# Kernel optimization log

Hardware: AMD Instinct MI355X
Metric: run time of the kernel (lower is better)

The kernel has to match this reference:

```python
import jax, jax.numpy as jnp
import numpy as np

# --- vocab metadata (replaces string itos_vocab lookups with precomputed tables) ---
# ids [0,128)   : pitch    'p0'..'p127'  (type 0)
# ids [128,289) : duration 'd0'..'d160'  (type 1)
# ids [289,390) : time     't0'..'t100'  (type 2)
# ids [390,518) : velocity 'v0'..'v127'  (type 3)
_tt = np.concatenate([np.full(128, 0), np.full(161, 1), np.full(101, 2), np.full(128, 3)]).astype(np.int32)
_tv = np.concatenate([np.arange(128), np.arange(161), np.arange(101), np.arange(128)]).astype(np.float32)
TOKEN_TYPE = jnp.asarray(_tt)   # [V]
TOKEN_VALUE = jnp.asarray(_tv)  # [V]
COEF = (1.0, 0.5, 0.5, 0.5, 0.5)  # matches init coeff_
# per-type numeric-distance normalizers (pitch unused: its branch is constant)
DENOM = jnp.array([1.0, 160.0, 100.0, 128.0], dtype=jnp.float32)
CW = jnp.array([COEF[1], COEF[2], COEF[3], COEF[4]], dtype=jnp.float32)

B, V, S = 32, 518, 2048


def setup_inputs() -> dict:
    key = jax.random.key(0)
    k1, k2 = jax.random.split(key)
    output = jax.random.normal(k1, (B, V, S), dtype=jnp.float32)  # logits [B, vocab, S]
    target = jax.random.randint(k2, (B, S), 0, V, dtype=jnp.int64)
    return {"output": output, "target": target}


def reference(output, target):
    target = target.astype(jnp.int32)
    # CrossEntropyLoss over class dim 1, mean over B*S
    lsm = jax.nn.log_softmax(output, axis=1)                       # [B,V,S]
    nll = -jnp.take_along_axis(lsm, target[:, None, :], axis=1)    # [B,1,S]
    loss = nll.mean()
    # faithful to source: softmax over last (sequence) dim, then argmax over vocab dim
    pred = jnp.argmax(jax.nn.softmax(output, axis=-1), axis=1)     # [B,S]
    pt, tt = TOKEN_TYPE[pred], TOKEN_TYPE[target]
    pv, tv = TOKEN_VALUE[pred], TOKEN_VALUE[target]
    diff = jnp.abs(pv - tv)
    # pitch branch: source compares 'pXX' != 'XX' which is always True -> constant coef[1]
    same_type = jnp.where(pt == 0, COEF[1], CW[pt] * diff / DENOM[pt])
    mask = jnp.where(pt != tt, COEF[0], same_type)                 # [B,S]
    high_cost = (loss * mask).mean()
    return loss + high_cost
```

## Files before the change

kernel.cpp:

```cpp
#include <hip/hip_runtime.h>

#define BV 518
#define SS 2048
#define NB 32
#define NCOL (NB * SS)

__device__ inline void tok_meta(int id, int& ty, float& val) {
    int base;
    if (id < 128)      { ty = 0; base = 0; }
    else if (id < 289) { ty = 1; base = 128; }
    else if (id < 390) { ty = 2; base = 289; }
    else               { ty = 3; base = 390; }
    val = (float)(id - base);
}

__global__ __launch_bounds__(256) void row_lse_kernel(const float* __restrict__ logits,
                                                      float* __restrict__ lse_row) {
    const int row = blockIdx.x;
    const float4* base4 = (const float4*)(logits + (size_t)row * SS);
    const int t = threadIdx.x;
    float4 x0 = base4[t];
    float4 x1 = base4[t + 256];
    float s = __expf(x0.x) + __expf(x0.y) + __expf(x0.z) + __expf(x0.w)
            + __expf(x1.x) + __expf(x1.y) + __expf(x1.z) + __expf(x1.w);
    #pragma unroll
    for (int off = 32; off; off >>= 1) s += __shfl_down(s, off);
    __shared__ float ws[4];
    if ((t & 63) == 0) ws[t >> 6] = s;
    __syncthreads();
    if (t == 0) lse_row[row] = __logf(ws[0] + ws[1] + ws[2] + ws[3]);
}

__global__ __launch_bounds__(256) void col_partial_kernel(const float* __restrict__ logits,
                                                          const float* __restrict__ lse_row,
                                                          float* __restrict__ pse,
                                                          float* __restrict__ pbs,
                                                          int*   __restrict__ pbi) {
    const int bid   = blockIdx.x;
    const int vh    = bid >> 8;
    const int b     = (bid >> 3) & 31;
    const int stile = bid & 7;
    const int t     = threadIdx.x;
    const int lane  = t & 63;
    const int part  = t >> 6;

    __shared__ float slse[BV];
    for (int i = t; i < BV; i += 256) slse[i] = lse_row[b * BV + i];
    __syncthreads();

    const int fidx = stile * 64 + lane;
    const float4* rowbase = (const float4*)(logits + (size_t)b * BV * SS);

    const int vbase = vh ? 259 : 0;
    const int vend  = vh ? BV  : 259;

    float4 se = make_float4(0.f, 0.f, 0.f, 0.f);
    float4 bs = make_float4(-1e30f, -1e30f, -1e30f, -1e30f);
    int bix = 0x7fffffff, biy = 0x7fffffff, biz = 0x7fffffff, biw = 0x7fffffff;

    #pragma unroll 4
    for (int v = vbase + part; v < vend; v += 4) {
        float4 x = rowbase[(size_t)v * (SS / 4) + fidx];
        float l = slse[v];
        se.x += __expf(x.x); se.y += __expf(x.y);
        se.z += __expf(x.z); se.w += __expf(x.w);
        float c0 = x.x - l, c1 = x.y - l, c2 = x.z - l, c3 = x.w - l;
        if (c0 > bs.x) { bs.x = c0; bix = v; }
        if (c1 > bs.y) { bs.y = c1; biy = v; }
        if (c2 > bs.z) { bs.z = c2; biz = v; }
        if (c3 > bs.w) { bs.w = c3; biw = v; }
    }

    __shared__ float cse[4][256];
    __shared__ float cbs[4][256];
    __shared__ int   cbi[4][256];
    const int sb = lane * 4;
    cse[part][sb]     = se.x;  cse[part][sb + 1] = se.y;
    cse[part][sb + 2] = se.z;  cse[part][sb + 3] = se.w;
    cbs[part][sb]     = bs.x;  cbs[part][sb + 1] = bs.y;
    cbs[part][sb + 2] = bs.z;  cbs[part][sb + 3] = bs.w;
    cbi[part][sb]     = bix;   cbi[part][sb + 1] = biy;
    cbi[part][sb + 2] = biz;   cbi[part][sb + 3] = biw;
    __syncthreads();

    float tot = 0.f, best = -1e30f;
    int   bi  = 0x7fffffff;
    #pragma unroll
    for (int p = 0; p < 4; ++p) {
        tot += cse[p][t];
        float s2 = cbs[p][t]; int i2 = cbi[p][t];
        if (s2 > best || (s2 == best && i2 < bi)) { best = s2; bi = i2; }
    }
    const int g = (b * 8 + stile) * 256 + t;
    pse[vh * NCOL + g] = tot;
    pbs[vh * NCOL + g] = best;
    pbi[vh * NCOL + g] = bi;
}

__global__ __launch_bounds__(256) void combine_kernel(const float* __restrict__ logits,
                                                      const int* __restrict__ target,
                                                      const float* __restrict__ pse,
                                                      const float* __restrict__ pbs,
                                                      const int* __restrict__ pbi,
                                                      float* __restrict__ acc) {
    const int t = threadIdx.x;
    const int g = blockIdx.x * 256 + t;
    const int b = g >> 11;
    const int s = g & 2047;

    float tot = pse[g] + pse[NCOL + g];
    float b0 = pbs[g];        int i0 = pbi[g];
    float b1 = pbs[NCOL + g]; int i1 = pbi[NCOL + g];
    int bi = (b1 > b0) ? i1 : i0;

    const int tgt = target[g];
    const float ot = logits[(size_t)(b * BV + tgt) * SS + s];
    float nll = __logf(tot) - ot;

    int pt_, tt_; float pv_, tv_;
    tok_meta(bi, pt_, pv_);
    tok_meta(tgt, tt_, tv_);
    float mask;
    if (pt_ != tt_) {
        mask = 1.0f;
    } else if (pt_ == 0) {
        mask = 0.5f;
    } else {
        float dn = (pt_ == 1) ? 160.f : ((pt_ == 2) ? 100.f : 128.f);
        mask = 0.5f * fabsf(pv_ - tv_) / dn;
    }

    #pragma unroll
    for (int off = 32; off; off >>= 1) {
        nll  += __shfl_down(nll, off);
        mask += __shfl_down(mask, off);
    }
    __shared__ float wn[4], wm[4];
    if ((t & 63) == 0) { wn[t >> 6] = nll; wm[t >> 6] = mask; }
    __syncthreads();
    if (t == 0) {
        atomicAdd(&acc[0], wn[0] + wn[1] + wn[2] + wn[3]);
        atomicAdd(&acc[1], wm[0] + wm[1] + wm[2] + wm[3]);
    }
}

__global__ void finalize_kernel(const float* __restrict__ acc, float* __restrict__ out) {
    const float invN = 1.0f / (float)(NB * SS);
    float loss = acc[0] * invN;
    float mm   = acc[1] * invN;
    out[0] = loss * (1.0f + mm);
}

extern "C" void kernel_launch(void* const* d_in, const int* in_sizes, int n_in,
                              void* d_out, int out_size, void* d_ws, size_t ws_size,
                              hipStream_t stream) {
    const float* logits = (const float*)d_in[0];
    const int*   target = (const int*)d_in[1];
    float* outp = (float*)d_out;

    float* acc     = (float*)d_ws;
    float* lse_row = (float*)d_ws + 64;
    float* pse     = (float*)d_ws + 17024;
    float* pbs     = pse + 2 * NCOL;
    int*   pbi     = (int*)(pbs + 2 * NCOL);

    hipMemsetAsync(d_ws, 0, 64, stream);
    row_lse_kernel<<<NB * BV, 256, 0, stream>>>(logits, lse_row);
    col_partial_kernel<<<512, 256, 0, stream>>>(logits, lse_row, pse, pbs, pbi);
    combine_kernel<<<NCOL / 256, 256, 0, stream>>>(logits, target, pse, pbs, pbi, acc);
    finalize_kernel<<<1, 1, 0, stream>>>(acc, outp);
}
```

Before: 223.5 us.

## Fuse all stages into one cooperative kernel with grid syncs

Replaces the four separate launches (row log-sum-exp, column partials, combine, finalize) with a single cooperative kernel of 1024 blocks that separates the phases with grid-wide syncs. The row LSE phase now assigns one wave per row instead of one block per row, and the column phase splits the vocab into four quarters instead of two, giving 1024 blocks rather than 512. The aim is to remove launch overhead and raise parallelism in the column pass. The cost is grid-sync overhead, a requirement that all blocks are co-resident, and a partial reduction that no longer breaks ties toward the lower index.

Result: slower. 546.2 us (+144.4%).

```diff
diff --git a/kernel.cpp b/kernel.cpp
--- a/kernel.cpp
+++ b/kernel.cpp
@@ -1,9 +1,14 @@
 #include <hip/hip_runtime.h>
+#include <hip/hip_cooperative_groups.h>
+
+namespace cg = cooperative_groups;
 
 #define BV 518
 #define SS 2048
 #define NB 32
 #define NCOL (NB * SS)
+#define NBLK 1024
+#define NTHR 256
 
 __device__ inline void tok_meta(int id, int& ty, float& val) {
     int base;
@@ -14,141 +19,150 @@
     val = (float)(id - base);
 }
 
-__global__ __launch_bounds__(256) void row_lse_kernel(const float* __restrict__ logits,
-                                                      float* __restrict__ lse_row) {
-    const int row = blockIdx.x;
-    const float4* base4 = (const float4*)(logits + (size_t)row * SS);
-    const int t = threadIdx.x;
-    float4 x0 = base4[t];
-    float4 x1 = base4[t + 256];
-    float s = __expf(x0.x) + __expf(x0.y) + __expf(x0.z) + __expf(x0.w)
-            + __expf(x1.x) + __expf(x1.y) + __expf(x1.z) + __expf(x1.w);
-    #pragma unroll
-    for (int off = 32; off; off >>= 1) s += __shfl_down(s, off);
-    __shared__ float ws[4];
-    if ((t & 63) == 0) ws[t >> 6] = s;
-    __syncthreads();
-    if (t == 0) lse_row[row] = __logf(ws[0] + ws[1] + ws[2] + ws[3]);
-}
+__global__ __launch_bounds__(NTHR, 4) void fused_kernel(const float* __restrict__ logits,
+                                                        const int* __restrict__ target,
+                                                        float* __restrict__ ws,
+                                                        float* __restrict__ out) {
+    float* acc     = ws;
+    float* lse_row = ws + 64;
+    float* pse     = ws + 64 + 16640;
+    float* pbs     = pse + 4 * NCOL;
+    int*   pbi     = (int*)(pbs + 4 * NCOL);
 
-__global__ __launch_bounds__(256) void col_partial_kernel(const float* __restrict__ logits,
-                                                          const float* __restrict__ lse_row,
-                                                          float* __restrict__ pse,
-                                                          float* __restrict__ pbs,
-                                                          int*   __restrict__ pbi) {
-    const int bid   = blockIdx.x;
-    const int vh    = bid >> 8;
-    const int b     = (bid >> 3) & 31;
-    const int stile = bid & 7;
-    const int t     = threadIdx.x;
-    const int lane  = t & 63;
-    const int part  = t >> 6;
-
-    __shared__ float slse[BV];
-    for (int i = t; i < BV; i += 256) slse[i] = lse_row[b * BV + i];
-    __syncthreads();
-
-    const int fidx = stile * 64 + lane;
-    const float4* rowbase = (const float4*)(logits + (size_t)b * BV * SS);
-
-    const int vbase = vh ? 259 : 0;
-    const int vend  = vh ? BV  : 259;
-
-    float4 se = make_float4(0.f, 0.f, 0.f, 0.f);
-    float4 bs = make_float4(-1e30f, -1e30f, -1e30f, -1e30f);
-    int bix = 0x7fffffff, biy = 0x7fffffff, biz = 0x7fffffff, biw = 0x7fffffff;
-
-    #pragma unroll 4
-    for (int v = vbase + part; v < vend; v += 4) {
-        float4 x = rowbase[(size_t)v * (SS / 4) + fidx];
-        float l = slse[v];
-        se.x += __expf(x.x); se.y += __expf(x.y);
-        se.z += __expf(x.z); se.w += __expf(x.w);
-        float c0 = x.x - l, c1 = x.y - l, c2 = x.z - l, c3 = x.w - l;
-        if (c0 > bs.x) { bs.x = c0; bix = v; }
-        if (c1 > bs.y) { bs.y = c1; biy = v; }
-        if (c2 > bs.z) { bs.z = c2; biz = v; }
-        if (c3 > bs.w) { bs.w = c3; biw = v; }
-    }
+    const int t   = threadIdx.x;
+    const int bid = blockIdx.x;
+    cg::grid_group grid = cg::this_grid();
 
     __shared__ float cse[4][256];
     __shared__ float cbs[4][256];
     __shared__ int   cbi[4][256];
-    const int sb = lane * 4;
-    cse[part][sb]     = se.x;  cse[part][sb + 1] = se.y;
-    cse[part][sb + 2] = se.z;  cse[part][sb + 3] = se.w;
-    cbs[part][sb]     = bs.x;  cbs[part][sb + 1] = bs.y;
-    cbs[part][sb + 2] = bs.z;  cbs[part][sb + 3] = bs.w;
-    cbi[part][sb]     = bix;   cbi[part][sb + 1] = biy;
-    cbi[part][sb + 2] = biz;   cbi[part][sb + 3] = biw;
-    __syncthreads();
+    __shared__ float slse[544];
 
-    float tot = 0.f, best = -1e30f;
-    int   bi  = 0x7fffffff;
-    #pragma unroll
-    for (int p = 0; p < 4; ++p) {
-        tot += cse[p][t];
-        float s2 = cbs[p][t]; int i2 = cbi[p][t];
-        if (s2 > best || (s2 == best && i2 < bi)) { best = s2; bi = i2; }
+    {
+        const int wave = bid * 4 + (t >> 6);
+        const int lane = t & 63;
+        for (int row = wave; row < NB * BV; row += 4 * NBLK) {
+            const float4* b4 = (const float4*)(logits + (size_t)row * SS);
+            float s = 0.f;
+            #pragma unroll
+            for (int i = 0; i < 8; ++i) {
+                float4 x = b4[lane + 64 * i];
+                s += __expf(x.x) + __expf(x.y) + __expf(x.z) + __expf(x.w);
+            }
+            #pragma unroll
+            for (int off = 32; off; off >>= 1) s += __shfl_down(s, off);
+            if (lane == 0) lse_row[row] = __logf(s);
+        }
     }
-    const int g = (b * 8 + stile) * 256 + t;
-    pse[vh * NCOL + g] = tot;
-    pbs[vh * NCOL + g] = best;
-    pbi[vh * NCOL + g] = bi;
-}
+    grid.sync();
 
-__global__ __launch_bounds__(256) void combine_kernel(const float* __restrict__ logits,
-                                                      const int* __restrict__ target,
-                                                      const float* __restrict__ pse,
-                                                      const float* __restrict__ pbs,
-                                                      const int* __restrict__ pbi,
-                                                      float* __restrict__ acc) {
-    const int t = threadIdx.x;
-    const int g = blockIdx.x * 256 + t;
-    const int b = g >> 11;
-    const int s = g & 2047;
+    {
+        const int q     = bid & 3;
+        const int stile = (bid >> 2) & 7;
+        const int b     = bid >> 5;
+        for (int i = t; i < BV; i += NTHR) slse[i] = lse_row[b * BV + i];
+        __syncthreads();
 
-    float tot = pse[g] + pse[NCOL + g];
-    float b0 = pbs[g];        int i0 = pbi[g];
-    float b1 = pbs[NCOL + g]; int i1 = pbi[NCOL + g];
-    int bi = (b1 > b0) ? i1 : i0;
+        const int lane = t & 63;
+        const int part = t >> 6;
+        const int fidx = stile * 64 + lane;
+        const float4* rowbase = (const float4*)(logits + (size_t)b * BV * SS);
 
-    const int tgt = target[g];
-    const float ot = logits[(size_t)(b * BV + tgt) * SS + s];
-    float nll = __logf(tot) - ot;
+        const int vqs = (BV * q) >> 2;
+        const int vqe = (BV * (q + 1)) >> 2;
 
-    int pt_, tt_; float pv_, tv_;
-    tok_meta(bi, pt_, pv_);
-    tok_meta(tgt, tt_, tv_);
-    float mask;
-    if (pt_ != tt_) {
-        mask = 1.0f;
-    } else if (pt_ == 0) {
-        mask = 0.5f;
-    } else {
-        float dn = (pt_ == 1) ? 160.f : ((pt_ == 2) ? 100.f : 128.f);
-        mask = 0.5f * fabsf(pv_ - tv_) / dn;
+        float4 se = make_float4(0.f, 0.f, 0.f, 0.f);
+        float4 bs = make_float4(-1e30f, -1e30f, -1e30f, -1e30f);
+        int bix = 0x7fffffff, biy = 0x7fffffff, biz = 0x7fffffff, biw = 0x7fffffff;
+
+        #pragma unroll 4
+        for (int v = vqs + part; v < vqe; v += 4) {
+            float4 x = rowbase[(size_t)v * (SS / 4) + fidx];
+            float l = slse[v];
+            se.x += __expf(x.x); se.y += __expf(x.y);
+            se.z += __expf(x.z); se.w += __expf(x.w);
+            float c0 = x.x - l, c1 = x.y - l, c2 = x.z - l, c3 = x.w - l;
+            if (c0 > bs.x) { bs.x = c0; bix = v; }
+            if (c1 > bs.y) { bs.y = c1; biy = v; }
+            if (c2 > bs.z) { bs.z = c2; biz = v; }
+            if (c3 > bs.w) { bs.w = c3; biw = v; }
+        }
+
+        const int sb = lane * 4;
+        cse[part][sb]     = se.x;  cse[part][sb + 1] = se.y;
+        cse[part][sb + 2] = se.z;  cse[part][sb + 3] = se.w;
+        cbs[part][sb]     = bs.x;  cbs[part][sb + 1] = bs.y;
+        cbs[part][sb + 2] = bs.z;  cbs[part][sb + 3] = bs.w;
+        cbi[part][sb]     = bix;   cbi[part][sb + 1] = biy;
+        cbi[part][sb + 2] = biz;   cbi[part][sb + 3] = biw;
+        __syncthreads();
+
+        float tot = 0.f, best = -1e30f;
+        int   bi  = 0x7fffffff;
+        #pragma unroll
+        for (int p = 0; p < 4; ++p) {
+            tot += cse[p][t];
+            float s2 = cbs[p][t]; int i2 = cbi[p][t];
+            if (s2 > best || (s2 == best && i2 < bi)) { best = s2; bi = i2; }
+        }
+        const int g = b * SS + stile * 256 + t;
+        pse[q * NCOL + g] = tot;
+        pbs[q * NCOL + g] = best;
+        pbi[q * NCOL + g] = bi;
     }
+    grid.sync();
 
-    #pragma unroll
-    for (int off = 32; off; off >>= 1) {
-        nll  += __shfl_down(nll, off);
-        mask += __shfl_down(mask, off);
+    if (bid < NCOL / NTHR) {
+        const int g = bid * NTHR + t;
+        const int b = g >> 11;
+        const int s = g & 2047;
+
+        float tot = 0.f, best = -1e30f;
+        int   bi  = 0x7fffffff;
+        #pragma unroll
+        for (int q = 0; q < 4; ++q) {
+            tot += pse[q * NCOL + g];
+            float s2 = pbs[q * NCOL + g]; int i2 = pbi[q * NCOL + g];
+            if (s2 > best) { best = s2; bi = i2; }
+        }
+
+        const int tgt = target[g];
+        const float ot = logits[(size_t)(b * BV + tgt) * SS + s];
+        float nll = __logf(tot) - ot;
+
+        int pt_, tt_; float pv_, tv_;
+        tok_meta(bi, pt_, pv_);
+        tok_meta(tgt, tt_, tv_);
+        float mask;
+        if (pt_ != tt_) {
+            mask = 1.0f;
+        } else if (pt_ == 0) {
+            mask = 0.5f;
+        } else {
+            float dn = (pt_ == 1) ? 160.f : ((pt_ == 2) ? 100.f : 128.f);
+            mask = 0.5f * fabsf(pv_ - tv_) / dn;
+        }
+
+        #pragma unroll
+        for (int off = 32; off; off >>= 1) {
+            nll  += __shfl_down(nll, off);
+            mask += __shfl_down(mask, off);
+        }
+        if ((t & 63) == 0) { cse[0][t >> 6] = nll; cbs[0][t >> 6] = mask; }
+        __syncthreads();
+        if (t == 0) {
+            atomicAdd(&acc[0], cse[0][0] + cse[0][1] + cse[0][2] + cse[0][3]);
+            atomicAdd(&acc[1], cbs[0][0] + cbs[0][1] + cbs[0][2] + cbs[0][3]);
+        }
     }
-    __shared__ float wn[4], wm[4];
-    if ((t & 63) == 0) { wn[t >> 6] = nll; wm[t >> 6] = mask; }
-    __syncthreads();
-    if (t == 0) {
-        atomicAdd(&acc[0], wn[0] + wn[1] + wn[2] + wn[3]);
-        atomicAdd(&acc[1], wm[0] + wm[1] + wm[2] + wm[3]);
+    grid.sync();
+
+    if (bid == 0 && t == 0) {
+        const float invN = 1.0f / (float)NCOL;
+        float loss = acc[0] * invN;
+        float mm   = acc[1] * invN;
+        out[0] = loss * (1.0f + mm);
     }
-}
-
-__global__ void finalize_kernel(const float* __restrict__ acc, float* __restrict__ out) {
-    const float invN = 1.0f / (float)(NB * SS);
-    float loss = acc[0] * invN;
-    float mm   = acc[1] * invN;
-    out[0] = loss * (1.0f + mm);
 }
 
 extern "C" void kernel_launch(void* const* d_in, const int* in_sizes, int n_in,
@@ -157,16 +171,11 @@
     const float* logits = (const float*)d_in[0];
     const int*   target = (const int*)d_in[1];
     float* outp = (float*)d_out;
-
-    float* acc     = (float*)d_ws;
-    float* lse_row = (float*)d_ws + 64;
-    float* pse     = (float*)d_ws + 17024;
-    float* pbs     = pse + 2 * NCOL;
-    int*   pbi     = (int*)(pbs + 2 * NCOL);
+    float* ws   = (float*)d_ws;
 
     hipMemsetAsync(d_ws, 0, 64, stream);
-    row_lse_kernel<<<NB * BV, 256, 0, stream>>>(logits, lse_row);
-    col_partial_kernel<<<512, 256, 0, stream>>>(logits, lse_row, pse, pbs, pbi);
-    combine_kernel<<<NCOL / 256, 256, 0, stream>>>(logits, target, pse, pbs, pbi, acc);
-    finalize_kernel<<<1, 1, 0, stream>>>(acc, outp);
+
+    void* args[] = { (void*)&logits, (void*)&target, (void*)&ws, (void*)&outp };
+    hipLaunchCooperativeKernel((const void*)fused_kernel, dim3(NBLK), dim3(NTHR),
+                               args, 0, stream);
 }
```

## Split vocab into eight chunks for column pass and software-prefetch loads

Applied to the files above, without the earlier changes.

The column-partial kernel now splits the vocabulary dimension into eight chunks instead of two, launching 2048 blocks instead of 512 so more of the GPU is busy. It adds explicit two-deep register prefetching of the next float4 rows and sets launch bounds for occupancy. The combine kernel now reduces eight partials per column, which adds partial-buffer writes and reads. Argmax tie-breaking across chunks uses strict greater-than, so the lower chunk wins on ties.

After: 223.6 us. About the same (+0.1%).

```diff
diff --git a/kernel.cpp b/kernel.cpp
--- a/kernel.cpp
+++ b/kernel.cpp
@@ -4,6 +4,7 @@
 #define SS 2048
 #define NB 32
 #define NCOL (NB * SS)
+#define NQ 8
 
 __device__ inline void tok_meta(int id, int& ty, float& val) {
     int base;
@@ -31,45 +32,64 @@
     if (t == 0) lse_row[row] = __logf(ws[0] + ws[1] + ws[2] + ws[3]);
 }
 
-__global__ __launch_bounds__(256) void col_partial_kernel(const float* __restrict__ logits,
-                                                          const float* __restrict__ lse_row,
-                                                          float* __restrict__ pse,
-                                                          float* __restrict__ pbs,
-                                                          int*   __restrict__ pbi) {
+__global__ __launch_bounds__(256, 8) void col_partial_kernel(const float* __restrict__ logits,
+                                                             const float* __restrict__ lse_row,
+                                                             float* __restrict__ pse,
+                                                             float* __restrict__ pbs,
+                                                             int*   __restrict__ pbi) {
     const int bid   = blockIdx.x;
-    const int vh    = bid >> 8;
-    const int b     = (bid >> 3) & 31;
-    const int stile = bid & 7;
+    const int q     = bid & 7;
+    const int stile = (bid >> 3) & 7;
+    const int b     = bid >> 6;
     const int t     = threadIdx.x;
     const int lane  = t & 63;
     const int part  = t >> 6;
 
-    __shared__ float slse[BV];
+    __shared__ float slse[544];
     for (int i = t; i < BV; i += 256) slse[i] = lse_row[b * BV + i];
     __syncthreads();
 
     const int fidx = stile * 64 + lane;
     const float4* rowbase = (const float4*)(logits + (size_t)b * BV * SS);
 
-    const int vbase = vh ? 259 : 0;
-    const int vend  = vh ? BV  : 259;
+    const int vqs = (BV * q) >> 3;
+    const int vqe = (BV * (q + 1)) >> 3;
 
     float4 se = make_float4(0.f, 0.f, 0.f, 0.f);
     float4 bs = make_float4(-1e30f, -1e30f, -1e30f, -1e30f);
     int bix = 0x7fffffff, biy = 0x7fffffff, biz = 0x7fffffff, biw = 0x7fffffff;
 
-    #pragma unroll 4
-    for (int v = vbase + part; v < vend; v += 4) {
-        float4 x = rowbase[(size_t)v * (SS / 4) + fidx];
-        float l = slse[v];
-        se.x += __expf(x.x); se.y += __expf(x.y);
-        se.z += __expf(x.z); se.w += __expf(x.w);
-        float c0 = x.x - l, c1 = x.y - l, c2 = x.z - l, c3 = x.w - l;
-        if (c0 > bs.x) { bs.x = c0; bix = v; }
-        if (c1 > bs.y) { bs.y = c1; biy = v; }
-        if (c2 > bs.z) { bs.z = c2; biz = v; }
-        if (c3 > bs.w) { bs.w = c3; biw = v; }
+#define PROC(X, V)                                                        \
+    {                                                                     \
+        float l = slse[(V)];                                              \
+        se.x += __expf((X).x); se.y += __expf((X).y);                     \
+        se.z += __expf((X).z); se.w += __expf((X).w);                     \
+        float c0 = (X).x - l, c1 = (X).y - l, c2 = (X).z - l, c3 = (X).w - l; \
+        if (c0 > bs.x) { bs.x = c0; bix = (V); }                          \
+        if (c1 > bs.y) { bs.y = c1; biy = (V); }                          \
+        if (c2 > bs.z) { bs.z = c2; biz = (V); }                          \
+        if (c3 > bs.w) { bs.w = c3; biw = (V); }                          \
     }
+
+    const int K = (vqe - vqs - part + 3) >> 2;
+    int v = vqs + part;
+    const int vlast = vqs + part + 4 * (K - 1);
+    float4 x0 = rowbase[(size_t)v * (SS / 4) + fidx];
+    int v1c = (v + 4 <= vlast) ? v + 4 : vlast;
+    float4 x1 = rowbase[(size_t)v1c * (SS / 4) + fidx];
+    int k = 0;
+    while (k + 2 <= K) {
+        int n0c = (v + 8  <= vlast) ? v + 8  : vlast;
+        int n1c = (v + 12 <= vlast) ? v + 12 : vlast;
+        float4 n0 = rowbase[(size_t)n0c * (SS / 4) + fidx];
+        float4 n1 = rowbase[(size_t)n1c * (SS / 4) + fidx];
+        PROC(x0, v);
+        PROC(x1, v + 4);
+        x0 = n0; x1 = n1;
+        v += 8; k += 2;
+    }
+    if (k < K) PROC(x0, v);
+#undef PROC
 
     __shared__ float cse[4][256];
     __shared__ float cbs[4][256];
@@ -91,10 +111,10 @@
         float s2 = cbs[p][t]; int i2 = cbi[p][t];
         if (s2 > best || (s2 == best && i2 < bi)) { best = s2; bi = i2; }
     }
-    const int g = (b * 8 + stile) * 256 + t;
-    pse[vh * NCOL + g] = tot;
-    pbs[vh * NCOL + g] = best;
-    pbi[vh * NCOL + g] = bi;
+    const int g = b * SS + stile * 256 + t;
+    pse[q * NCOL + g] = tot;
+    pbs[q * NCOL + g] = best;
+    pbi[q * NCOL + g] = bi;
 }
 
 __global__ __launch_bounds__(256) void combine_kernel(const float* __restrict__ logits,
@@ -108,10 +128,14 @@
     const int b = g >> 11;
     const int s = g & 2047;
 
-    float tot = pse[g] + pse[NCOL + g];
-    float b0 = pbs[g];        int i0 = pbi[g];
-    float b1 = pbs[NCOL + g]; int i1 = pbi[NCOL + g];
-    int bi = (b1 > b0) ? i1 : i0;
+    float tot = 0.f, best = -1e30f;
+    int   bi  = 0x7fffffff;
+    #pragma unroll
+    for (int q = 0; q < NQ; ++q) {
+        tot += pse[q * NCOL + g];
+        float s2 = pbs[q * NCOL + g]; int i2 = pbi[q * NCOL + g];
+        if (s2 > best) { best = s2; bi = i2; }
+    }
 
     const int tgt = target[g];
     const float ot = logits[(size_t)(b * BV + tgt) * SS + s];
@@ -160,13 +184,13 @@
 
     float* acc     = (float*)d_ws;
     float* lse_row = (float*)d_ws + 64;
-    float* pse     = (float*)d_ws + 17024;
-    float* pbs     = pse + 2 * NCOL;
-    int*   pbi     = (int*)(pbs + 2 * NCOL);
+    float* pse     = (float*)d_ws + 64 + 16640;
+    float* pbs     = pse + NQ * NCOL;
+    int*   pbi     = (int*)(pbs + NQ * NCOL);
 
     hipMemsetAsync(d_ws, 0, 64, stream);
     row_lse_kernel<<<NB * BV, 256, 0, stream>>>(logits, lse_row);
-    col_partial_kernel<<<512, 256, 0, stream>>>(logits, lse_row, pse, pbs, pbi);
+    col_partial_kernel<<<NB * 64, 256, 0, stream>>>(logits, lse_row, pse, pbs, pbi);
     combine_kernel<<<NCOL / 256, 256, 0, stream>>>(logits, target, pse, pbs, pbi, acc);
     finalize_kernel<<<1, 1, 0, stream>>>(acc, outp);
 }
```
